# Optimization experiments

Hardware: AMD Instinct MI355X
Metric: run time of the kernel (lower is better)

## Reference

```python
import jax, jax.numpy as jnp
import numpy as np

BH = 32  # block_h
BW = 32  # block_w
M, K, N = 4096, 4096, 4096  # tokens, in_features, out_features


def setup_inputs() -> dict:
    key = jax.random.key(0)
    k1, k2, k3, k4 = jax.random.split(key, 4)
    data = jax.random.normal(k1, (M, K), dtype=jnp.float32)
    weight = jax.random.normal(k2, (N, K), dtype=jnp.float32) * 0.02
    bias = jax.random.normal(k3, (N,), dtype=jnp.float32) * 0.02
    # elementwise 0/1 mask over the weight matrix
    mask = jax.random.randint(k4, (N, K), 0, 2, dtype=jnp.int32)
    # conv bias of the 1x1-channel block-summing conv; chosen so ~half the
    # 32x32 blocks (sum ~ Binomial(1024, 0.5)) end up inactive
    conv_bias = jnp.full((1,), -512.0, dtype=jnp.float32)
    return {"data": data, "weight": weight, "bias": bias, "mask": mask,
            "conv_bias": conv_bias}


def reference(data, weight, bias, mask, conv_bias):
    n_out, n_in = weight.shape
    nH, nW = n_out // BH, n_in // BW
    # conv2d with all-ones (BH,BW) kernel, stride (BH,BW) == per-block sum + bias
    block_sum = mask.astype(jnp.float32).reshape(nH, BH, nW, BW).sum(axis=(1, 3))
    block_mask = (block_sum + conv_bias[0]) > 0  # [nH, nW] bool
    # dds matmul (trans_b=True): zero inactive weight blocks, out = data @ W^T
    w_blocks = weight.reshape(nH, BH, nW, BW)
    w_masked = (w_blocks * block_mask[:, None, :, None].astype(weight.dtype)
                ).reshape(n_out, n_in)
    out = jnp.einsum('mk,nk->mn', data, w_masked) + bias
    return out
```

## Files before the change

kernel.cpp:

```cpp
#include <hip/hip_runtime.h>
#include <hip/hip_bf16.h>
#include <stdint.h>

#define M_DIM 4096
#define N_DIM 4096
#define K_DIM 4096
#define NH 128
#define NW 128
#define NKT 64

typedef short bf16x8 __attribute__((ext_vector_type(8)));
typedef short bf16x4 __attribute__((ext_vector_type(4)));
typedef float f32x4 __attribute__((ext_vector_type(4)));

#define MFMA(a, b, c) __builtin_amdgcn_mfma_f32_16x16x32_bf16((a), (b), (c), 0, 0, 0)

__device__ __forceinline__ short f2bf(float f) {
  union { float f; unsigned u; } c; c.f = f;
  unsigned u = c.u;
  unsigned r = (u + 0x7fffu + ((u >> 16) & 1u)) >> 16;
  return (short)r;
}

__global__ __launch_bounds__(256) void k_block_mask(const int* __restrict__ mask,
                                                    const float* __restrict__ conv_bias,
                                                    int* __restrict__ bm) {
  const int bw = blockIdx.x, bh = blockIdx.y;
  const int t = threadIdx.x;
  const int row = t >> 3;
  const int c4 = (t & 7) << 2;
  const int4* p = (const int4*)(mask + (size_t)(bh * 32 + row) * K_DIM + bw * 32 + c4);
  int4 v = *p;
  int s = v.x + v.y + v.z + v.w;
#pragma unroll
  for (int off = 32; off > 0; off >>= 1) s += __shfl_down(s, off);
  __shared__ int red[4];
  if ((t & 63) == 0) red[t >> 6] = s;
  __syncthreads();
  if (t == 0) {
    float tot = (float)(red[0] + red[1] + red[2] + red[3]) + conv_bias[0];
    bm[bh * NW + bw] = (tot > 0.0f) ? 1 : 0;
  }
}

__global__ __launch_bounds__(256) void k_cvt_data(const float* __restrict__ in,
                                                  short* __restrict__ ob) {
  size_t i = (size_t)blockIdx.x * 256 + threadIdx.x;
  f32x4 v = ((const f32x4*)in)[i];
  bf16x4 o;
  o[0] = f2bf(v[0]); o[1] = f2bf(v[1]); o[2] = f2bf(v[2]); o[3] = f2bf(v[3]);
  ((bf16x4*)ob)[i] = o;
}

__global__ __launch_bounds__(256) void k_cvt_weight(const float* __restrict__ w,
                                                    const int* __restrict__ bm,
                                                    short* __restrict__ ob) {
  size_t i = (size_t)blockIdx.x * 256 + threadIdx.x;
  int n = (int)(i >> 10);
  int k = ((int)i & 1023) << 2;
  float m = bm[((n >> 5) << 7) + (k >> 5)] ? 1.0f : 0.0f;
  f32x4 v = ((const f32x4*)w)[i];
  bf16x4 o;
  o[0] = f2bf(v[0] * m); o[1] = f2bf(v[1] * m);
  o[2] = f2bf(v[2] * m); o[3] = f2bf(v[3] * m);
  ((bf16x4*)ob)[i] = o;
}

__global__ __launch_bounds__(512, 2) void k_gemm256(const short* __restrict__ Ab,
                                                    const short* __restrict__ Bb,
                                                    const float* __restrict__ bias,
                                                    float* __restrict__ out) {
  __shared__ short Asm[2][2][256][32];
  __shared__ short Bsm[2][2][256][32];

  const int tid = threadIdx.x;
  const int wid = tid >> 6, lane = tid & 63;
  const int wr = wid >> 2, wc = wid & 3;
  const int r = lane & 15, g0 = lane >> 4;
  const int gs = g0 ^ ((r >> 1) & 3);

  const int swz = (blockIdx.x & 7) * 32 + (blockIdx.x >> 3);
  const int bx = swz & 15, by = swz >> 4;
  const int rowM = by * 256, colN = bx * 256;

  const int srow = tid >> 2;
  const int sseg = (tid & 3) ^ ((tid >> 3) & 3);
  const int swave = wid * 512;

  const short* gA = Ab + (size_t)(rowM + srow) * K_DIM + sseg * 8;
  const short* gB = Bb + (size_t)(colN + srow) * K_DIM + sseg * 8;
  const size_t HOFF = (size_t)128 * K_DIM;

#define GLL(g, l)                                                            \
  __builtin_amdgcn_global_load_lds((const __attribute__((address_space(1))) void*)(g), \
                                   (__attribute__((address_space(3))) void*)(l), 16, 0, 0)
#define STA(BUF, kt, h, ks) GLL(gA + HOFF * (h) + (size_t)(kt) * 64 + (ks) * 32, \
                                &Asm[BUF][ks][(h) * 128][0] + swave)
#define STB(BUF, kt, h, ks) GLL(gB + HOFF * (h) + (size_t)(kt) * 64 + (ks) * 32, \
                                &Bsm[BUF][ks][(h) * 128][0] + swave)

#define LDA(BUF, ks, m) (*(const bf16x8*)&Asm[BUF][ks][wr * 128 + (m) * 16 + r][gs * 8])
#define LDB(BUF, ks, n) (*(const bf16x8*)&Bsm[BUF][ks][wc * 64 + (n) * 16 + r][gs * 8])
#define LDA8(BUF, ks)                                                        \
  a[0] = LDA(BUF, ks, 0); a[1] = LDA(BUF, ks, 1); a[2] = LDA(BUF, ks, 2);    \
  a[3] = LDA(BUF, ks, 3); a[4] = LDA(BUF, ks, 4); a[5] = LDA(BUF, ks, 5);    \
  a[6] = LDA(BUF, ks, 6); a[7] = LDA(BUF, ks, 7);
#define MF8(nn, bb)                                                          \
  acc[0][nn] = MFMA(a[0], bb, acc[0][nn]); acc[1][nn] = MFMA(a[1], bb, acc[1][nn]); \
  acc[2][nn] = MFMA(a[2], bb, acc[2][nn]); acc[3][nn] = MFMA(a[3], bb, acc[3][nn]); \
  acc[4][nn] = MFMA(a[4], bb, acc[4][nn]); acc[5][nn] = MFMA(a[5], bb, acc[5][nn]); \
  acc[6][nn] = MFMA(a[6], bb, acc[6][nn]); acc[7][nn] = MFMA(a[7], bb, acc[7][nn]);
#define BAR __builtin_amdgcn_s_barrier()
#define PRIO1 __builtin_amdgcn_s_setprio(1)
#define PRIO0 __builtin_amdgcn_s_setprio(0)

#define TILE(BUF, NB, u, SB, SA, VM)                                         \
  {                                                                          \
    bf16x8 a[8], p, q;                                                       \
    LDA8(BUF, 0);                                                            \
    p = LDB(BUF, 0, 0); q = LDB(BUF, 0, 1);                                  \
    if (SB) { STB(NB, (u) + 1, 0, 0); STB(NB, (u) + 1, 0, 1); }              \
    BAR; PRIO1; MF8(0, p); MF8(1, q); PRIO0; BAR;                            \
    p = LDB(BUF, 0, 2); q = LDB(BUF, 0, 3);                                  \
    if (SB) { STB(NB, (u) + 1, 1, 0); STB(NB, (u) + 1, 1, 1); }              \
    BAR; PRIO1; MF8(2, p); MF8(3, q); PRIO0; BAR;                            \
    LDA8(BUF, 1);                                                            \
    p = LDB(BUF, 1, 0); q = LDB(BUF, 1, 1);                                  \
    if (SA) { STA(BUF, (u) + 2, 0, 0); STA(BUF, (u) + 2, 1, 0); }            \
    BAR; PRIO1; MF8(0, p); MF8(1, q); PRIO0; BAR;                            \
    p = LDB(BUF, 1, 2); q = LDB(BUF, 1, 3);                                  \
    if (SA) { STA(BUF, (u) + 2, 0, 1); STA(BUF, (u) + 2, 1, 1); }            \
    BAR; PRIO1; MF8(2, p); MF8(3, q); PRIO0;                                 \
    asm volatile("s_waitcnt vmcnt(" #VM ")" ::: "memory");                   \
    BAR;                                                                     \
  }

  f32x4 acc[8][4];
#pragma unroll
  for (int m = 0; m < 8; ++m)
#pragma unroll
    for (int n = 0; n < 4; ++n) acc[m][n] = (f32x4){0.f, 0.f, 0.f, 0.f};

  STA(0, 0, 0, 0); STA(0, 0, 1, 0); STA(0, 0, 0, 1); STA(0, 0, 1, 1);
  STB(0, 0, 0, 0); STB(0, 0, 1, 0); STB(0, 0, 0, 1); STB(0, 0, 1, 1);
  STA(1, 1, 0, 0); STA(1, 1, 1, 0); STA(1, 1, 0, 1); STA(1, 1, 1, 1);
  asm volatile("s_waitcnt vmcnt(4)" ::: "memory");
  BAR;

#pragma unroll 1
  for (int u = 0; u < NKT - 2; u += 2) {
    TILE(0, 1, u, 1, 1, 4);
    TILE(1, 0, u + 1, 1, 1, 4);
  }
  TILE(0, 1, NKT - 2, 1, 0, 0);
  TILE(1, 0, NKT - 1, 0, 0, 0);

  const int orow = rowM + wr * 128;
  const int ocol = colN + wc * 64;
#pragma unroll
  for (int n = 0; n < 4; ++n) {
    int col = ocol + n * 16 + r;
    float bz = bias[col];
#pragma unroll
    for (int m = 0; m < 8; ++m) {
      int row0 = orow + m * 16 + g0 * 4;
#pragma unroll
      for (int j = 0; j < 4; ++j)
        out[(size_t)(row0 + j) * N_DIM + col] = acc[m][n][j] + bz;
    }
  }
#undef TILE
#undef GLL
#undef STA
#undef STB
#undef LDA
#undef LDB
#undef LDA8
#undef MF8
#undef BAR
#undef PRIO1
#undef PRIO0
}

__global__ __launch_bounds__(256) void k_naive(const float* __restrict__ A,
                                               const float* __restrict__ W,
                                               const float* __restrict__ bias,
                                               const int* __restrict__ bm,
                                               float* __restrict__ out) {
  int col = blockIdx.x * 16 + (threadIdx.x & 15);
  int row = blockIdx.y * 16 + (threadIdx.x >> 4);
  float s = 0.f;
  for (int kb = 0; kb < K_DIM / 32; ++kb) {
    if (bm[(col >> 5) * NW + kb]) {
      int kbase = kb * 32;
#pragma unroll 8
      for (int k = 0; k < 32; ++k)
        s += A[(size_t)row * K_DIM + kbase + k] * W[(size_t)col * K_DIM + kbase + k];
    }
  }
  out[(size_t)row * N_DIM + col] = s + bias[col];
}

extern "C" void kernel_launch(void* const* d_in, const int* in_sizes, int n_in,
                              void* d_out, int out_size, void* d_ws, size_t ws_size,
                              hipStream_t stream) {
  const float* data = (const float*)d_in[0];
  const float* weight = (const float*)d_in[1];
  const float* bias = (const float*)d_in[2];
  const int* mask = (const int*)d_in[3];
  const float* conv_bias = (const float*)d_in[4];
  float* out = (float*)d_out;

  int* bm = (int*)d_ws;
  const size_t off_a = 65536;
  const size_t off_b = off_a + (size_t)M_DIM * K_DIM * 2;
  const size_t needed = off_b + (size_t)N_DIM * K_DIM * 2;

  k_block_mask<<<dim3(NW, NH), 256, 0, stream>>>(mask, conv_bias, bm);

  if (ws_size >= needed) {
    short* Abf = (short*)((char*)d_ws + off_a);
    short* Wbf = (short*)((char*)d_ws + off_b);
    k_cvt_data<<<dim3((M_DIM * (K_DIM / 4)) / 256), 256, 0, stream>>>(data, Abf);
    k_cvt_weight<<<dim3((N_DIM * (K_DIM / 4)) / 256), 256, 0, stream>>>(weight, bm, Wbf);
    k_gemm256<<<dim3(256), 512, 0, stream>>>(Abf, Wbf, bias, out);
  } else {
    k_naive<<<dim3(N_DIM / 16, M_DIM / 16), 256, 0, stream>>>(data, weight, bias, bm, out);
  }
}
```

Measured before the change: 177.4 us.

## Software-pipeline LDS fragment loads one phase ahead with double-buffered registers

Restructures the per-tile GEMM loop so LDS reads for the next MFMA phase, including the next tile's first A/B fragments, are issued before the current phase's MFMAs. Two register sets (aX/aY, bA/bB) ping-pong, and sched_barriers pin the instruction order. Barriers and vmcnt waits are rearranged to match, so LDS read latency overlaps with matrix math. The cost is more VGPRs for the extra A fragments, which may hurt occupancy or cause spills, plus tighter reasoning about buffer reuse hazards.

```diff
diff --git a/kernel.cpp b/kernel.cpp
--- a/kernel.cpp
+++ b/kernel.cpp
@@ -101,38 +101,54 @@
 
 #define LDA(BUF, ks, m) (*(const bf16x8*)&Asm[BUF][ks][wr * 128 + (m) * 16 + r][gs * 8])
 #define LDB(BUF, ks, n) (*(const bf16x8*)&Bsm[BUF][ks][wc * 64 + (n) * 16 + r][gs * 8])
-#define LDA8(BUF, ks)                                                        \
-  a[0] = LDA(BUF, ks, 0); a[1] = LDA(BUF, ks, 1); a[2] = LDA(BUF, ks, 2);    \
-  a[3] = LDA(BUF, ks, 3); a[4] = LDA(BUF, ks, 4); a[5] = LDA(BUF, ks, 5);    \
-  a[6] = LDA(BUF, ks, 6); a[7] = LDA(BUF, ks, 7);
-#define MF8(nn, bb)                                                          \
-  acc[0][nn] = MFMA(a[0], bb, acc[0][nn]); acc[1][nn] = MFMA(a[1], bb, acc[1][nn]); \
-  acc[2][nn] = MFMA(a[2], bb, acc[2][nn]); acc[3][nn] = MFMA(a[3], bb, acc[3][nn]); \
-  acc[4][nn] = MFMA(a[4], bb, acc[4][nn]); acc[5][nn] = MFMA(a[5], bb, acc[5][nn]); \
-  acc[6][nn] = MFMA(a[6], bb, acc[6][nn]); acc[7][nn] = MFMA(a[7], bb, acc[7][nn]);
+
+#define MF8(AR, nn, bb)                                                      \
+  acc[0][nn] = MFMA(AR[0], bb, acc[0][nn]); acc[1][nn] = MFMA(AR[1], bb, acc[1][nn]); \
+  acc[2][nn] = MFMA(AR[2], bb, acc[2][nn]); acc[3][nn] = MFMA(AR[3], bb, acc[3][nn]); \
+  acc[4][nn] = MFMA(AR[4], bb, acc[4][nn]); acc[5][nn] = MFMA(AR[5], bb, acc[5][nn]); \
+  acc[6][nn] = MFMA(AR[6], bb, acc[6][nn]); acc[7][nn] = MFMA(AR[7], bb, acc[7][nn]);
+
 #define BAR __builtin_amdgcn_s_barrier()
+#define SB0 __builtin_amdgcn_sched_barrier(0)
 #define PRIO1 __builtin_amdgcn_s_setprio(1)
 #define PRIO0 __builtin_amdgcn_s_setprio(0)
-
-#define TILE(BUF, NB, u, SB, SA, VM)                                         \
+#define VMW_(N) asm volatile("s_waitcnt vmcnt(" #N ")" ::: "memory")
+#define VMW(N) VMW_(N)
+
+#define TILE(BUF, NB, u, SB, SA, SR, VM0, VM2)                               \
   {                                                                          \
-    bf16x8 a[8], p, q;                                                       \
-    LDA8(BUF, 0);                                                            \
-    p = LDB(BUF, 0, 0); q = LDB(BUF, 0, 1);                                  \
-    if (SB) { STB(NB, (u) + 1, 0, 0); STB(NB, (u) + 1, 0, 1); }              \
-    BAR; PRIO1; MF8(0, p); MF8(1, q); PRIO0; BAR;                            \
-    p = LDB(BUF, 0, 2); q = LDB(BUF, 0, 3);                                  \
-    if (SB) { STB(NB, (u) + 1, 1, 0); STB(NB, (u) + 1, 1, 1); }              \
-    BAR; PRIO1; MF8(2, p); MF8(3, q); PRIO0; BAR;                            \
-    LDA8(BUF, 1);                                                            \
-    p = LDB(BUF, 1, 0); q = LDB(BUF, 1, 1);                                  \
+                                               \
+    BAR; SB0;                                                                \
+    bB[0] = LDB(BUF, 0, 2); bB[1] = LDB(BUF, 0, 3);                          \
+    aY[0] = LDA(BUF, 1, 0); aY[1] = LDA(BUF, 1, 1);                          \
+    aY[2] = LDA(BUF, 1, 2); aY[3] = LDA(BUF, 1, 3);                          \
+    PRIO1; MF8(aX, 0, bA[0]); MF8(aX, 1, bA[1]); PRIO0;                      \
+    if (SB) { STB(NB, (u) + 1, 0, 0); STB(NB, (u) + 1, 1, 0); }              \
+    VMW(VM0);                                                                \
+                                               \
+    BAR; SB0;                                                                \
+    aY[4] = LDA(BUF, 1, 4); aY[5] = LDA(BUF, 1, 5);                          \
+    aY[6] = LDA(BUF, 1, 6); aY[7] = LDA(BUF, 1, 7);                          \
+    bA[0] = LDB(BUF, 1, 0); bA[1] = LDB(BUF, 1, 1);                          \
+    PRIO1; MF8(aX, 2, bB[0]); MF8(aX, 3, bB[1]); PRIO0;                      \
+    if (SB) { STB(NB, (u) + 1, 0, 1); STB(NB, (u) + 1, 1, 1); }              \
+                                               \
+    BAR; SB0;                                                                \
+    bB[0] = LDB(BUF, 1, 2); bB[1] = LDB(BUF, 1, 3);                          \
+    PRIO1; MF8(aY, 0, bA[0]); MF8(aY, 1, bA[1]); PRIO0;                      \
     if (SA) { STA(BUF, (u) + 2, 0, 0); STA(BUF, (u) + 2, 1, 0); }            \
-    BAR; PRIO1; MF8(0, p); MF8(1, q); PRIO0; BAR;                            \
-    p = LDB(BUF, 1, 2); q = LDB(BUF, 1, 3);                                  \
+    VMW(VM2);                                                                \
+       \
+    BAR; SB0;                                                                \
+    if (SR) {                                                                \
+      aX[0] = LDA(NB, 0, 0); aX[1] = LDA(NB, 0, 1);                          \
+      aX[2] = LDA(NB, 0, 2); aX[3] = LDA(NB, 0, 3);                          \
+      aX[4] = LDA(NB, 0, 4); aX[5] = LDA(NB, 0, 5);                          \
+      aX[6] = LDA(NB, 0, 6); aX[7] = LDA(NB, 0, 7);                          \
+      bA[0] = LDB(NB, 0, 0); bA[1] = LDB(NB, 0, 1);                          \
+    }                                                                        \
+    PRIO1; MF8(aY, 2, bB[0]); MF8(aY, 3, bB[1]); PRIO0;                      \
     if (SA) { STA(BUF, (u) + 2, 0, 1); STA(BUF, (u) + 2, 1, 1); }            \
-    BAR; PRIO1; MF8(2, p); MF8(3, q); PRIO0;                                 \
-    asm volatile("s_waitcnt vmcnt(" #VM ")" ::: "memory");                   \
-    BAR;                                                                     \
   }
 
   f32x4 acc[8][4];
@@ -140,20 +156,26 @@
   for (int m = 0; m < 8; ++m)
 #pragma unroll
     for (int n = 0; n < 4; ++n) acc[m][n] = (f32x4){0.f, 0.f, 0.f, 0.f};
+
+  bf16x8 aX[8], aY[8], bA[2], bB[2];
 
   STA(0, 0, 0, 0); STA(0, 0, 1, 0); STA(0, 0, 0, 1); STA(0, 0, 1, 1);
   STB(0, 0, 0, 0); STB(0, 0, 1, 0); STB(0, 0, 0, 1); STB(0, 0, 1, 1);
   STA(1, 1, 0, 0); STA(1, 1, 1, 0); STA(1, 1, 0, 1); STA(1, 1, 1, 1);
-  asm volatile("s_waitcnt vmcnt(4)" ::: "memory");
-  BAR;
+  VMW(4);
+  BAR; SB0;
+  aX[0] = LDA(0, 0, 0); aX[1] = LDA(0, 0, 1); aX[2] = LDA(0, 0, 2);
+  aX[3] = LDA(0, 0, 3); aX[4] = LDA(0, 0, 4); aX[5] = LDA(0, 0, 5);
+  aX[6] = LDA(0, 0, 6); aX[7] = LDA(0, 0, 7);
+  bA[0] = LDB(0, 0, 0); bA[1] = LDB(0, 0, 1);
 
 #pragma unroll 1
   for (int u = 0; u < NKT - 2; u += 2) {
-    TILE(0, 1, u, 1, 1, 4);
-    TILE(1, 0, u + 1, 1, 1, 4);
-  }
-  TILE(0, 1, NKT - 2, 1, 0, 0);
-  TILE(1, 0, NKT - 1, 0, 0, 0);
+    TILE(0, 1, u, 1, 1, 1, 6, 4);
+    TILE(1, 0, u + 1, 1, 1, 1, 6, 4);
+  }
+  TILE(0, 1, NKT - 2, 1, 0, 1, 6, 2);
+  TILE(1, 0, NKT - 1, 0, 0, 0, 0, 0);
 
   const int orow = rowM + wr * 128;
   const int ocol = colN + wc * 64;
@@ -175,11 +197,13 @@
 #undef STB
 #undef LDA
 #undef LDB
-#undef LDA8
 #undef MF8
 #undef BAR
+#undef SB0
 #undef PRIO1
 #undef PRIO0
+#undef VMW
+#undef VMW_
 }
 
 __global__ __launch_bounds__(256) void k_naive(const float* __restrict__ A,
```

Measured after the change: 160.1 us. -9.8%, faster.

## Fuse block-mask into weight conversion and skip inactive blocks in GEMM

Applied to the files above, without the earlier changes.

Merges the block-mask reduction with weight bf16 conversion so inactive weight blocks are never read, only zero-written. The GEMM is restructured to 128x256 tiles with K-step 32 and a triple-buffered LDS pipeline. Each wave ballots its block-mask bits and skips MFMAs and LDS reads for inactive 32x32 weight blocks. Global loads still run for every tile, so the memory traffic into LDS is unchanged, and the smaller tile lowers data reuse while the per-wave branching adds control overhead.

```diff
diff --git a/kernel.cpp b/kernel.cpp
--- a/kernel.cpp
+++ b/kernel.cpp
@@ -7,7 +7,7 @@
 #define K_DIM 4096
 #define NH 128
 #define NW 128
-#define NKT 64
+#define NKT2 128
 
 typedef short bf16x8 __attribute__((ext_vector_type(8)));
 typedef short bf16x4 __attribute__((ext_vector_type(4)));
@@ -22,25 +22,41 @@
   return (short)r;
 }
 
-__global__ __launch_bounds__(256) void k_block_mask(const int* __restrict__ mask,
-                                                    const float* __restrict__ conv_bias,
-                                                    int* __restrict__ bm) {
+__global__ __launch_bounds__(256) void k_mask_weight(const int* __restrict__ mask,
+                                                     const float* __restrict__ conv_bias,
+                                                     const float* __restrict__ w,
+                                                     int* __restrict__ bm,
+                                                     short* __restrict__ ob) {
   const int bw = blockIdx.x, bh = blockIdx.y;
   const int t = threadIdx.x;
   const int row = t >> 3;
   const int c4 = (t & 7) << 2;
-  const int4* p = (const int4*)(mask + (size_t)(bh * 32 + row) * K_DIM + bw * 32 + c4);
-  int4 v = *p;
+  const size_t off = (size_t)(bh * 32 + row) * K_DIM + bw * 32 + c4;
+
+  int4 v = *(const int4*)(mask + off);
   int s = v.x + v.y + v.z + v.w;
 #pragma unroll
-  for (int off = 32; off > 0; off >>= 1) s += __shfl_down(s, off);
+  for (int o = 32; o > 0; o >>= 1) s += __shfl_down(s, o);
   __shared__ int red[4];
+  __shared__ int active;
   if ((t & 63) == 0) red[t >> 6] = s;
   __syncthreads();
   if (t == 0) {
     float tot = (float)(red[0] + red[1] + red[2] + red[3]) + conv_bias[0];
-    bm[bh * NW + bw] = (tot > 0.0f) ? 1 : 0;
-  }
+    int a = (tot > 0.0f) ? 1 : 0;
+    bm[bh * NW + bw] = a;
+    active = a;
+  }
+  __syncthreads();
+
+  bf16x4 o;
+  if (active) {
+    f32x4 wv = *(const f32x4*)(w + off);
+    o[0] = f2bf(wv[0]); o[1] = f2bf(wv[1]); o[2] = f2bf(wv[2]); o[3] = f2bf(wv[3]);
+  } else {
+    o[0] = 0; o[1] = 0; o[2] = 0; o[3] = 0;
+  }
+  *(bf16x4*)(ob + off) = o;
 }
 
 __global__ __launch_bounds__(256) void k_cvt_data(const float* __restrict__ in,
@@ -52,26 +68,13 @@
   ((bf16x4*)ob)[i] = o;
 }
 
-__global__ __launch_bounds__(256) void k_cvt_weight(const float* __restrict__ w,
-                                                    const int* __restrict__ bm,
-                                                    short* __restrict__ ob) {
-  size_t i = (size_t)blockIdx.x * 256 + threadIdx.x;
-  int n = (int)(i >> 10);
-  int k = ((int)i & 1023) << 2;
-  float m = bm[((n >> 5) << 7) + (k >> 5)] ? 1.0f : 0.0f;
-  f32x4 v = ((const f32x4*)w)[i];
-  bf16x4 o;
-  o[0] = f2bf(v[0] * m); o[1] = f2bf(v[1] * m);
-  o[2] = f2bf(v[2] * m); o[3] = f2bf(v[3] * m);
-  ((bf16x4*)ob)[i] = o;
-}
-
 __global__ __launch_bounds__(512, 2) void k_gemm256(const short* __restrict__ Ab,
                                                     const short* __restrict__ Bb,
                                                     const float* __restrict__ bias,
+                                                    const int* __restrict__ bm,
                                                     float* __restrict__ out) {
-  __shared__ short Asm[2][2][256][32];
-  __shared__ short Bsm[2][2][256][32];
+  __shared__ short Asm[3][128][32];
+  __shared__ short Bsm[3][256][32];
 
   const int tid = threadIdx.x;
   const int wid = tid >> 6, lane = tid & 63;
@@ -79,9 +82,9 @@
   const int r = lane & 15, g0 = lane >> 4;
   const int gs = g0 ^ ((r >> 1) & 3);
 
-  const int swz = (blockIdx.x & 7) * 32 + (blockIdx.x >> 3);
+  const int swz = (blockIdx.x & 7) * 64 + (blockIdx.x >> 3);
   const int bx = swz & 15, by = swz >> 4;
-  const int rowM = by * 256, colN = bx * 256;
+  const int rowM = by * 128, colN = bx * 256;
 
   const int srow = tid >> 2;
   const int sseg = (tid & 3) ^ ((tid >> 3) & 3);
@@ -91,78 +94,81 @@
   const short* gB = Bb + (size_t)(colN + srow) * K_DIM + sseg * 8;
   const size_t HOFF = (size_t)128 * K_DIM;
 
+  const int nb0 = (colN >> 5) + wc * 2;
+  const int* bp = bm + (size_t)nb0 * NW;
+  unsigned long long w0l = __ballot(bp[lane] != 0);
+  unsigned long long w0h = __ballot(bp[64 + lane] != 0);
+  unsigned long long w1l = __ballot(bp[NW + lane] != 0);
+  unsigned long long w1h = __ballot(bp[NW + 64 + lane] != 0);
+  __builtin_amdgcn_sched_barrier(0);
+
 #define GLL(g, l)                                                            \
   __builtin_amdgcn_global_load_lds((const __attribute__((address_space(1))) void*)(g), \
                                    (__attribute__((address_space(3))) void*)(l), 16, 0, 0)
-#define STA(BUF, kt, h, ks) GLL(gA + HOFF * (h) + (size_t)(kt) * 64 + (ks) * 32, \
-                                &Asm[BUF][ks][(h) * 128][0] + swave)
-#define STB(BUF, kt, h, ks) GLL(gB + HOFF * (h) + (size_t)(kt) * 64 + (ks) * 32, \
-                                &Bsm[BUF][ks][(h) * 128][0] + swave)
-
-#define LDA(BUF, ks, m) (*(const bf16x8*)&Asm[BUF][ks][wr * 128 + (m) * 16 + r][gs * 8])
-#define LDB(BUF, ks, n) (*(const bf16x8*)&Bsm[BUF][ks][wc * 64 + (n) * 16 + r][gs * 8])
-#define LDA8(BUF, ks)                                                        \
-  a[0] = LDA(BUF, ks, 0); a[1] = LDA(BUF, ks, 1); a[2] = LDA(BUF, ks, 2);    \
-  a[3] = LDA(BUF, ks, 3); a[4] = LDA(BUF, ks, 4); a[5] = LDA(BUF, ks, 5);    \
-  a[6] = LDA(BUF, ks, 6); a[7] = LDA(BUF, ks, 7);
-#define MF8(nn, bb)                                                          \
-  acc[0][nn] = MFMA(a[0], bb, acc[0][nn]); acc[1][nn] = MFMA(a[1], bb, acc[1][nn]); \
-  acc[2][nn] = MFMA(a[2], bb, acc[2][nn]); acc[3][nn] = MFMA(a[3], bb, acc[3][nn]); \
-  acc[4][nn] = MFMA(a[4], bb, acc[4][nn]); acc[5][nn] = MFMA(a[5], bb, acc[5][nn]); \
-  acc[6][nn] = MFMA(a[6], bb, acc[6][nn]); acc[7][nn] = MFMA(a[7], bb, acc[7][nn]);
+#define STA(SBUF, kt) GLL(gA + (size_t)(kt) * 32, &Asm[SBUF][0][0] + swave)
+#define STBH(SBUF, kt, h) GLL(gB + HOFF * (h) + (size_t)(kt) * 32, \
+                              &Bsm[SBUF][(h) * 128][0] + swave)
+
+#define LDA(BUF, m) (*(const bf16x8*)&Asm[BUF][wr * 64 + (m) * 16 + r][gs * 8])
+#define LDB(BUF, n) (*(const bf16x8*)&Bsm[BUF][wc * 64 + (n) * 16 + r][gs * 8])
+
+#define MF4(bb, n)                                                           \
+  acc[0][n] = MFMA(aX0, bb, acc[0][n]); acc[1][n] = MFMA(aX1, bb, acc[1][n]); \
+  acc[2][n] = MFMA(aX2, bb, acc[2][n]); acc[3][n] = MFMA(aX3, bb, acc[3][n]);
+
 #define BAR __builtin_amdgcn_s_barrier()
+#define SB0 __builtin_amdgcn_sched_barrier(0)
 #define PRIO1 __builtin_amdgcn_s_setprio(1)
 #define PRIO0 __builtin_amdgcn_s_setprio(0)
-
-#define TILE(BUF, NB, u, SB, SA, VM)                                         \
+#define VMW_(N) asm volatile("s_waitcnt vmcnt(" #N ")" ::: "memory")
+#define VMW(N) VMW_(N)
+
+#define TILE(BUF, SBUF, u, SG, VM)                                           \
   {                                                                          \
-    bf16x8 a[8], p, q;                                                       \
-    LDA8(BUF, 0);                                                            \
-    p = LDB(BUF, 0, 0); q = LDB(BUF, 0, 1);                                  \
-    if (SB) { STB(NB, (u) + 1, 0, 0); STB(NB, (u) + 1, 0, 1); }              \
-    BAR; PRIO1; MF8(0, p); MF8(1, q); PRIO0; BAR;                            \
-    p = LDB(BUF, 0, 2); q = LDB(BUF, 0, 3);                                  \
-    if (SB) { STB(NB, (u) + 1, 1, 0); STB(NB, (u) + 1, 1, 1); }              \
-    BAR; PRIO1; MF8(2, p); MF8(3, q); PRIO0; BAR;                            \
-    LDA8(BUF, 1);                                                            \
-    p = LDB(BUF, 1, 0); q = LDB(BUF, 1, 1);                                  \
-    if (SA) { STA(BUF, (u) + 2, 0, 0); STA(BUF, (u) + 2, 1, 0); }            \
-    BAR; PRIO1; MF8(0, p); MF8(1, q); PRIO0; BAR;                            \
-    p = LDB(BUF, 1, 2); q = LDB(BUF, 1, 3);                                  \
-    if (SA) { STA(BUF, (u) + 2, 0, 1); STA(BUF, (u) + 2, 1, 1); }            \
-    BAR; PRIO1; MF8(2, p); MF8(3, q); PRIO0;                                 \
-    asm volatile("s_waitcnt vmcnt(" #VM ")" ::: "memory");                   \
-    BAR;                                                                     \
-  }
-
-  f32x4 acc[8][4];
-#pragma unroll
-  for (int m = 0; m < 8; ++m)
+    const int kb = (u);                                                      \
+    const int e0 = (int)((((kb) & 64) ? w0h : w0l) >> ((kb) & 63)) & 1;      \
+    const int e1 = (int)((((kb) & 64) ? w1h : w1l) >> ((kb) & 63)) & 1;      \
+    bf16x8 aX0, aX1, aX2, aX3, b0, b1, b2, b3;                               \
+    if (e0 | e1) { aX0 = LDA(BUF, 0); aX1 = LDA(BUF, 1);                     \
+                   aX2 = LDA(BUF, 2); aX3 = LDA(BUF, 3); }                   \
+    if (e0) { b0 = LDB(BUF, 0); b1 = LDB(BUF, 1); }                          \
+    if (e1) { b2 = LDB(BUF, 2); b3 = LDB(BUF, 3); }                          \
+    if (SG) { STA(SBUF, (u) + 2); STBH(SBUF, (u) + 2, 0); STBH(SBUF, (u) + 2, 1); } \
+    PRIO1;                                                                   \
+    if (e0) { MF4(b0, 0) MF4(b1, 1) }                                        \
+    if (e1) { MF4(b2, 2) MF4(b3, 3) }                                        \
+    PRIO0;                                                                   \
+    VMW(VM); BAR; SB0;                                                       \
+  }
+
+  f32x4 acc[4][4];
+#pragma unroll
+  for (int m = 0; m < 4; ++m)
 #pragma unroll
     for (int n = 0; n < 4; ++n) acc[m][n] = (f32x4){0.f, 0.f, 0.f, 0.f};
 
-  STA(0, 0, 0, 0); STA(0, 0, 1, 0); STA(0, 0, 0, 1); STA(0, 0, 1, 1);
-  STB(0, 0, 0, 0); STB(0, 0, 1, 0); STB(0, 0, 0, 1); STB(0, 0, 1, 1);
-  STA(1, 1, 0, 0); STA(1, 1, 1, 0); STA(1, 1, 0, 1); STA(1, 1, 1, 1);
-  asm volatile("s_waitcnt vmcnt(4)" ::: "memory");
-  BAR;
+  STA(0, 0); STBH(0, 0, 0); STBH(0, 0, 1);
+  STA(1, 1); STBH(1, 1, 0); STBH(1, 1, 1);
+  VMW(3);
+  BAR; SB0;
 
 #pragma unroll 1
-  for (int u = 0; u < NKT - 2; u += 2) {
-    TILE(0, 1, u, 1, 1, 4);
-    TILE(1, 0, u + 1, 1, 1, 4);
-  }
-  TILE(0, 1, NKT - 2, 1, 0, 0);
-  TILE(1, 0, NKT - 1, 0, 0, 0);
-
-  const int orow = rowM + wr * 128;
+  for (int u = 0; u < 126; u += 3) {
+    TILE(0, 2, u, 1, 3);
+    TILE(1, 0, u + 1, 1, 3);
+    TILE(2, 1, u + 2, 1, 3);
+  }
+  TILE(0, 0, 126, 0, 0);
+  TILE(1, 0, 127, 0, 0);
+
+  const int orow = rowM + wr * 64;
   const int ocol = colN + wc * 64;
 #pragma unroll
   for (int n = 0; n < 4; ++n) {
     int col = ocol + n * 16 + r;
     float bz = bias[col];
 #pragma unroll
-    for (int m = 0; m < 8; ++m) {
+    for (int m = 0; m < 4; ++m) {
       int row0 = orow + m * 16 + g0 * 4;
 #pragma unroll
       for (int j = 0; j < 4; ++j)
@@ -172,14 +178,16 @@
 #undef TILE
 #undef GLL
 #undef STA
-#undef STB
+#undef STBH
 #undef LDA
 #undef LDB
-#undef LDA8
-#undef MF8
+#undef MF4
 #undef BAR
+#undef SB0
 #undef PRIO1
 #undef PRIO0
+#undef VMW
+#undef VMW_
 }
 
 __global__ __launch_bounds__(256) void k_naive(const float* __restrict__ A,
@@ -201,6 +209,27 @@
   out[(size_t)row * N_DIM + col] = s + bias[col];
 }
 
+__global__ __launch_bounds__(256) void k_block_mask(const int* __restrict__ mask,
+                                                    const float* __restrict__ conv_bias,
+                                                    int* __restrict__ bm) {
+  const int bw = blockIdx.x, bh = blockIdx.y;
+  const int t = threadIdx.x;
+  const int row = t >> 3;
+  const int c4 = (t & 7) << 2;
+  const int4* p = (const int4*)(mask + (size_t)(bh * 32 + row) * K_DIM + bw * 32 + c4);
+  int4 v = *p;
+  int s = v.x + v.y + v.z + v.w;
+#pragma unroll
+  for (int off = 32; off > 0; off >>= 1) s += __shfl_down(s, off);
+  __shared__ int red[4];
+  if ((t & 63) == 0) red[t >> 6] = s;
+  __syncthreads();
+  if (t == 0) {
+    float tot = (float)(red[0] + red[1] + red[2] + red[3]) + conv_bias[0];
+    bm[bh * NW + bw] = (tot > 0.0f) ? 1 : 0;
+  }
+}
+
 extern "C" void kernel_launch(void* const* d_in, const int* in_sizes, int n_in,
                               void* d_out, int out_size, void* d_ws, size_t ws_size,
                               hipStream_t stream) {
@@ -216,15 +245,14 @@
   const size_t off_b = off_a + (size_t)M_DIM * K_DIM * 2;
   const size_t needed = off_b + (size_t)N_DIM * K_DIM * 2;
 
-  k_block_mask<<<dim3(NW, NH), 256, 0, stream>>>(mask, conv_bias, bm);
-
   if (ws_size >= needed) {
     short* Abf = (short*)((char*)d_ws + off_a);
     short* Wbf = (short*)((char*)d_ws + off_b);
+    k_mask_weight<<<dim3(NW, NH), 256, 0, stream>>>(mask, conv_bias, weight, bm, Wbf);
     k_cvt_data<<<dim3((M_DIM * (K_DIM / 4)) / 256), 256, 0, stream>>>(data, Abf);
-    k_cvt_weight<<<dim3((N_DIM * (K_DIM / 4)) / 256), 256, 0, stream>>>(weight, bm, Wbf);
-    k_gemm256<<<dim3(256), 512, 0, stream>>>(Abf, Wbf, bias, out);
+    k_gemm256<<<dim3(512), 512, 0, stream>>>(Abf, Wbf, bias, bm, out);
   } else {
+    k_block_mask<<<dim3(NW, NH), 256, 0, stream>>>(mask, conv_bias, bm);
     k_naive<<<dim3(N_DIM / 16, M_DIM / 16), 256, 0, stream>>>(data, weight, bias, bm, out);
   }
 }
```

New measurement: 182.9 us. 1.03x slower.
